# Kernel optimization log

Measured on AMD Instinct MI355X. Metric: run time of the kernel, lower is better.

## Reference

```python
import jax, jax.numpy as jnp
import numpy as np

B, T, D, K = 4, 4096, 256, 16


def hankel_eigvecs(T: int, k: int) -> jnp.ndarray:
    """Top-k |eigenvalue| eigenvectors of Z_ij = 2/((i+j)^3 - (i+j)), 1-indexed."""
    idx = np.arange(1, T + 1, dtype=np.float64)
    ij = idx[None, :] + idx[:, None]
    Z = 2.0 / (ij ** 3 - ij)
    w, v = np.linalg.eigh(Z)
    top = np.argsort(-np.abs(w))[:k]
    return jnp.asarray(v[:, top], dtype=jnp.float32)  # (T, K)


def setup_inputs() -> dict:
    key = jax.random.key(0)
    kx, kw = jax.random.split(key)
    x = jax.random.normal(kx, (B, T, D), dtype=jnp.float32)
    # Stacked weights of the K independent nn.Linear(D, D, bias=False) modules.
    # W[k] is the torch Linear weight (out, in); y = c @ W[k].T.
    W = jax.random.normal(kw, (K, D, D), dtype=jnp.float32) * (1.0 / np.sqrt(D))
    phi = hankel_eigvecs(T, K)  # Hankel eigenvector buffer (non-trainable)
    return {"x": x, "W": W, "phi": phi}


def reference(x, W, phi):
    # x: (B,T,D), W: (K,D,D), phi: (T,K)
    # c_k[t] = cumsum_{s<=t} phi[s,k] * x[s]   -> batched over all K filters
    C = jnp.cumsum(phi[None, :, :, None] * x[:, :, None, :], axis=1)  # (B,T,K,D)
    # out[t] = sum_k phi[t,k] * (c_k[t] @ W_k^T)
    out = jnp.einsum('btkd,ked,tk->bte', C, W, phi)  # (B,T,D)
    return out  # dropout is identity in eval mode (dropout=0.0)
```

## Files before the change

kernel.cpp:

```cpp
#include <hip/hip_runtime.h>


typedef __bf16 bf16x8 __attribute__((ext_vector_type(8)));
typedef float  f32x4  __attribute__((ext_vector_type(4)));
typedef unsigned short u16;

__device__ static inline u16 f2bf(float f) {
    unsigned int u = __float_as_uint(f);
    u = (u + 0x7fffu + ((u >> 16) & 1u)) >> 16;
    return (u16)u;
}

__device__ static inline void gload16(const void* g, void* l) {
    __builtin_amdgcn_global_load_lds((const __attribute__((address_space(1))) void*)g,
                                     (__attribute__((address_space(3))) void*)l, 16, 0, 0);
}

__global__ __launch_bounds__(256) void k0_wt(const float* __restrict__ W, u16* __restrict__ WT) {
    const int e = blockIdx.x, d = threadIdx.x;
    union { u16 u[16]; uint4 v[2]; } ob;
#pragma unroll
    for (int k = 0; k < 16; ++k)
        ob.u[k] = f2bf(W[((size_t)k * 256 + e) * 256 + d]);
    uint4* dst = (uint4*)(WT + (size_t)e * 4096 + d * 16);
    dst[0] = ob.v[0]; dst[1] = ob.v[1];
}

__global__ __launch_bounds__(256) void k1_sums(const float* __restrict__ x,
                                               const float* __restrict__ phi,
                                               float* __restrict__ U) {
    __shared__ float phis[256];
    const int tid = threadIdx.x;
    const int b = blockIdx.x, c = blockIdx.y;
    const int t0 = c * 16;
    phis[tid] = phi[t0 * 16 + tid];
    __syncthreads();
    float acc[16];
#pragma unroll
    for (int k = 0; k < 16; ++k) acc[k] = 0.f;
    for (int s = 0; s < 16; ++s) {
        const float xv = x[(size_t)((b << 12) + t0 + s) * 256 + tid];
        union { float f[16]; float4 v[4]; } pv;
#pragma unroll
        for (int j = 0; j < 4; ++j) pv.v[j] = *(const float4*)&phis[s * 16 + j * 4];
#pragma unroll
        for (int k = 0; k < 16; ++k) acc[k] = fmaf(pv.f[k], xv, acc[k]);
    }
    float4* Up = (float4*)(U + ((size_t)((b * 256 + c) * 256 + tid)) * 16);
    union { float f[16]; float4 v[4]; } ov;
#pragma unroll
    for (int k = 0; k < 16; ++k) ov.f[k] = acc[k];
#pragma unroll
    for (int j = 0; j < 4; ++j) Up[j] = ov.v[j];
}

__global__ __launch_bounds__(256) void k2_scan(float* __restrict__ U) {
    const int b  = blockIdx.x;
    const int dl = threadIdx.x & 63;
    const int dk = blockIdx.y * 64 + dl;
    const int q  = threadIdx.x >> 6;
    float* base = U + (size_t)b * 1048576 + (size_t)(q * 64) * 4096 + dk;
    float s = 0.f;
#pragma unroll 8
    for (int j = 0; j < 64; ++j) s += base[(size_t)j * 4096];
    __shared__ float qs[4][64];
    qs[q][dl] = s;
    __syncthreads();
    float pre = 0.f;
#pragma unroll
    for (int i = 0; i < 4; ++i) pre += (i < q) ? qs[i][dl] : 0.f;
    float run = pre;
#pragma unroll 8
    for (int j = 0; j < 64; ++j) {
        const float v = base[(size_t)j * 4096];
        base[(size_t)j * 4096] = run;
        run += v;
    }
}

__global__ __launch_bounds__(512, 4) void k4_fused(const float* __restrict__ x,
                                                   const float* __restrict__ phi,
                                                   const float* __restrict__ U,
                                                   const u16* __restrict__ BT,
                                                   float* __restrict__ C) {
    __shared__ __align__(16) char smem[81920];
    const int tid = threadIdx.x;
    const int m0 = blockIdx.x * 64;
    const int ks = blockIdx.y;
    const int b  = m0 >> 12, t0 = m0 & 4095, c0 = t0 >> 4;
    const int w = tid >> 6, l = tid & 63;
    const int wm = (w >> 2) * 32, wn = (w & 3) * 64;
    const int lg = l >> 4, lr = l & 15;
    f32x4 acc[2][4] = {};

    float p[16];
    if (w < 4) {
#pragma unroll
        for (int s = 0; s < 16; ++s) p[s] = phi[(t0 + w * 16 + s) * 16 + lr];
    }
    const char* Bb = (const char*)BT;
    const int tl = tid & 255;
    const int colb = (lg * 16 + lr) * 2;

    auto stageB = [&](int kt, int buf) {
        const int kofs = ks * 4096 + kt * 128;
#pragma unroll
        for (int c = 0; c < 8; ++c) {
            const int row = c * 32 + (tl >> 3);
            gload16(Bb + (size_t)row * 8192 + kofs + (((tl & 7) * 16) ^ ((row & 7) << 4)),
                    smem + 16384 + buf * 32768 + c * 4096 + tl * 16);
        }
    };
    auto chains = [&](int kt, int buf) {
        const int d = ks * 128 + kt * 4 + lg;
        float run = U[(((size_t)(b * 256 + c0 + w)) * 256 + d) * 16 + lr];
        char* Ab = smem + buf * 8192 + w * 2048;
#pragma unroll
        for (int s = 0; s < 16; ++s) {
            const float xv = x[(size_t)(m0 + w * 16 + s) * 256 + d];
            run = fmaf(p[s], xv, run);
            *(u16*)(Ab + s * 128 + (colb ^ ((s & 7) << 4))) = f2bf(p[s] * run);
        }
    };

    if (w >= 4) stageB(0, 0); else chains(0, 0);
    __syncthreads();

    for (int kt = 0; kt < 32; ++kt) {
        const int cur = kt & 1;
        if (kt < 31) {
            if (w >= 4) stageB(kt + 1, cur ^ 1);
            else        chains(kt + 1, cur ^ 1);
        }
        const char* Abase = smem + cur * 8192;
        const char* Bbase = smem + 16384 + cur * 32768;
#pragma unroll
        for (int kk = 0; kk < 2; ++kk) {
            const int kb = kk * 64 + lg * 16;
            bf16x8 af[2], bfv[4];
#pragma unroll
            for (int mi = 0; mi < 2; ++mi) {
                const int r = wm + mi * 16 + lr;
                af[mi] = *(const bf16x8*)(Abase + r * 128 + (kb ^ ((r & 7) << 4)));
            }
#pragma unroll
            for (int ni = 0; ni < 4; ++ni) {
                const int n = wn + ni * 16 + lr;
                bfv[ni] = *(const bf16x8*)(Bbase + n * 128 + (kb ^ ((n & 7) << 4)));
            }
#pragma unroll
            for (int mi = 0; mi < 2; ++mi)
#pragma unroll
                for (int ni = 0; ni < 4; ++ni)
                    acc[mi][ni] = __builtin_amdgcn_mfma_f32_16x16x32_bf16(af[mi], bfv[ni], acc[mi][ni], 0, 0, 0);
        }
        __syncthreads();
    }

#pragma unroll
    for (int mi = 0; mi < 2; ++mi)
#pragma unroll
        for (int ni = 0; ni < 4; ++ni)
#pragma unroll
            for (int r = 0; r < 4; ++r) {
                const int row = m0 + wm + mi * 16 + lg * 4 + r;
                const int col = wn + ni * 16 + lr;
                unsafeAtomicAdd(&C[(size_t)row * 256 + col], acc[mi][ni][r]);
            }
}

extern "C" void kernel_launch(void* const* d_in, const int* in_sizes, int n_in,
                              void* d_out, int out_size, void* d_ws, size_t ws_size,
                              hipStream_t stream) {
    const float* x   = (const float*)d_in[0];
    const float* W   = (const float*)d_in[1];
    const float* phi = (const float*)d_in[2];
    float* out = (float*)d_out;

    char* ws = (char*)d_ws;
    u16*   WT = (u16*)ws;
    float* U  = (float*)(ws + (2u << 20));

    k0_wt  <<<256, 256, 0, stream>>>(W, WT);
    k1_sums<<<dim3(4, 256), 256, 0, stream>>>(x, phi, U);
    k2_scan<<<dim3(4, 64), 256, 0, stream>>>(U);
    hipMemsetAsync(d_out, 0, (size_t)out_size * sizeof(float), stream);
    k4_fused<<<dim3(256, 2), 512, 0, stream>>>(x, phi, U, WT, out);
}
```

Before: 98.70 us.

## Drop split-K, triple-buffer B, prefetch x chains and store output directly

Removes the two-way split-K grid so each block computes the full K=4096 reduction, which lets the output be written with plain stores instead of atomics and drops the memset. B tiles are now triple-buffered with manual vmcnt waits and raw barriers. Only two waves build the A chains, each thread handling two filter columns with packed bf16 conversion, and x loads are prefetched two steps ahead in registers. The cost is half the blocks (256), more LDS per block and lower occupancy, and the hand-placed waitcnt and barrier logic is fragile.

```diff
diff --git a/kernel.cpp b/kernel.cpp
--- a/kernel.cpp
+++ b/kernel.cpp
@@ -4,6 +4,7 @@
 typedef __bf16 bf16x8 __attribute__((ext_vector_type(8)));
 typedef float  f32x4  __attribute__((ext_vector_type(4)));
 typedef unsigned short u16;
+typedef unsigned int   u32;
 
 __device__ static inline u16 f2bf(float f) {
     unsigned int u = __float_as_uint(f);
@@ -78,62 +79,67 @@
     }
 }
 
-__global__ __launch_bounds__(512, 4) void k4_fused(const float* __restrict__ x,
+__global__ __launch_bounds__(512, 2) void k4_fused(const float* __restrict__ x,
                                                    const float* __restrict__ phi,
                                                    const float* __restrict__ U,
                                                    const u16* __restrict__ BT,
                                                    float* __restrict__ C) {
-    __shared__ __align__(16) char smem[81920];
+    __shared__ __align__(16) char smem[114688];
     const int tid = threadIdx.x;
     const int m0 = blockIdx.x * 64;
-    const int ks = blockIdx.y;
     const int b  = m0 >> 12, t0 = m0 & 4095, c0 = t0 >> 4;
     const int w = tid >> 6, l = tid & 63;
     const int wm = (w >> 2) * 32, wn = (w & 3) * 64;
     const int lg = l >> 4, lr = l & 15;
     f32x4 acc[2][4] = {};
 
-    float p[16];
-    if (w < 4) {
-#pragma unroll
-        for (int s = 0; s < 16; ++s) p[s] = phi[(t0 + w * 16 + s) * 16 + lr];
-    }
-    const char* Bb = (const char*)BT;
+    const bool is_chain = (w < 2);
+    const bool is_stage = (w >= 4);
+
+    const int kp = l & 7, dl = (l >> 3) & 3, ch = ((w & 1) << 1) | (l >> 5);
+    const int colb = dl * 32 + kp * 4;
+    float2 p01[16];
+    if (is_chain) {
+#pragma unroll
+        for (int s = 0; s < 16; ++s)
+            p01[s] = *(const float2*)&phi[(t0 + ch * 16 + s) * 16 + kp * 2];
+    }
+
     const int tl = tid & 255;
-    const int colb = (lg * 16 + lr) * 2;
-
-    auto stageB = [&](int kt, int buf) {
-        const int kofs = ks * 4096 + kt * 128;
-#pragma unroll
-        for (int c = 0; c < 8; ++c) {
-            const int row = c * 32 + (tl >> 3);
-            gload16(Bb + (size_t)row * 8192 + kofs + (((tl & 7) * 16) ^ ((row & 7) << 4)),
-                    smem + 16384 + buf * 32768 + c * 4096 + tl * 16);
-        }
-    };
-    auto chains = [&](int kt, int buf) {
-        const int d = ks * 128 + kt * 4 + lg;
-        float run = U[(((size_t)(b * 256 + c0 + w)) * 256 + d) * 16 + lr];
-        char* Ab = smem + buf * 8192 + w * 2048;
+    const char* bsrc = (const char*)BT + (size_t)(tl >> 3) * 8192
+                     + (((tl & 7) * 16) ^ (((tl >> 3) & 7) << 4));
+    char* const smemA = smem + 98304;
+
+    auto stageB = [&](int kt, int bufw) {
+        char* dst = smem + bufw * 32768 + tl * 16;
+        const char* src = bsrc + (size_t)kt * 128;
+#pragma unroll
+        for (int c = 0; c < 8; ++c)
+            gload16(src + (size_t)c * 262144, dst + c * 4096);
+    };
+    auto issueX = [&](float (&xr)[16], float2& us, int kt) {
+        const int d = kt * 4 + dl;
+        const float* xp = x + (size_t)(m0 + ch * 16) * 256 + d;
+#pragma unroll
+        for (int s = 0; s < 16; ++s) xr[s] = xp[(size_t)s * 256];
+        us = *(const float2*)&U[((size_t)((b * 256 + c0 + ch) * 256 + d)) * 16 + kp * 2];
+    };
+    auto chains = [&](const float (&xr)[16], float2 us, int abw) {
+        float r0 = us.x, r1 = us.y;
+        char* Ab = smemA + abw * 8192 + ch * 2048;
 #pragma unroll
         for (int s = 0; s < 16; ++s) {
-            const float xv = x[(size_t)(m0 + w * 16 + s) * 256 + d];
-            run = fmaf(p[s], xv, run);
-            *(u16*)(Ab + s * 128 + (colb ^ ((s & 7) << 4))) = f2bf(p[s] * run);
-        }
-    };
-
-    if (w >= 4) stageB(0, 0); else chains(0, 0);
-    __syncthreads();
-
-    for (int kt = 0; kt < 32; ++kt) {
-        const int cur = kt & 1;
-        if (kt < 31) {
-            if (w >= 4) stageB(kt + 1, cur ^ 1);
-            else        chains(kt + 1, cur ^ 1);
-        }
-        const char* Abase = smem + cur * 8192;
-        const char* Bbase = smem + 16384 + cur * 32768;
+            r0 = fmaf(p01[s].x, xr[s], r0);
+            r1 = fmaf(p01[s].y, xr[s], r1);
+            const float v0 = p01[s].x * r0, v1 = p01[s].y * r1;
+            u32 pk;
+            asm("v_cvt_pk_bf16_f32 %0, %1, %2" : "=v"(pk) : "v"(v0), "v"(v1));
+            *(u32*)(Ab + s * 128 + (colb ^ ((s & 7) << 4))) = pk;
+        }
+    };
+    auto mfma_phase = [&](int abr, int bbr) {
+        const char* Abase = smemA + abr * 8192;
+        const char* Bbase = smem + bbr * 32768;
 #pragma unroll
         for (int kk = 0; kk < 2; ++kk) {
             const int kb = kk * 64 + lg * 16;
@@ -154,7 +160,45 @@
                 for (int ni = 0; ni < 4; ++ni)
                     acc[mi][ni] = __builtin_amdgcn_mfma_f32_16x16x32_bf16(af[mi], bfv[ni], acc[mi][ni], 0, 0, 0);
         }
-        __syncthreads();
+    };
+
+    float xA[16], xB[16]; float2 uA, uB;
+    if (is_chain) { issueX(xA, uA, 0); issueX(xB, uB, 1); }
+    if (is_stage) { stageB(0, 0); stageB(1, 1); }
+    __builtin_amdgcn_sched_barrier(0);
+    if (is_chain) {
+        chains(xA, uA, 0);
+        asm volatile("s_waitcnt lgkmcnt(0)" ::: "memory");
+    }
+    if (is_stage) asm volatile("s_waitcnt vmcnt(8)" ::: "memory");
+    asm volatile("s_barrier" ::: "memory");
+
+    int br = 0, bw = 2;
+    auto body = [&](int kt, float (&xW)[16], float2& uW,
+                    const float (&xR)[16], float2 uR) {
+        const int abr = kt & 1;
+        if (kt + 2 < 64) {
+            if (is_stage)      stageB(kt + 2, bw);
+            else if (is_chain) issueX(xW, uW, kt + 2);
+        }
+        __builtin_amdgcn_sched_barrier(0);
+        if (is_chain && (kt + 1 < 64)) chains(xR, uR, abr ^ 1);
+        __builtin_amdgcn_s_setprio(1);
+        mfma_phase(abr, br);
+        __builtin_amdgcn_s_setprio(0);
+        if (is_chain) asm volatile("s_waitcnt lgkmcnt(0)" ::: "memory");
+        if (is_stage) {
+            if (kt + 2 < 64) asm volatile("s_waitcnt vmcnt(8)" ::: "memory");
+            else             asm volatile("s_waitcnt vmcnt(0)" ::: "memory");
+        }
+        if (kt < 63) asm volatile("s_barrier" ::: "memory");
+        br = (br == 2) ? 0 : br + 1;
+        bw = (bw == 2) ? 0 : bw + 1;
+    };
+
+    for (int kt = 0; kt < 64; kt += 2) {
+        body(kt,     xA, uA, xB, uB);
+        body(kt + 1, xB, uB, xA, uA);
     }
 
 #pragma unroll
@@ -165,7 +209,7 @@
             for (int r = 0; r < 4; ++r) {
                 const int row = m0 + wm + mi * 16 + lg * 4 + r;
                 const int col = wn + ni * 16 + lr;
-                unsafeAtomicAdd(&C[(size_t)row * 256 + col], acc[mi][ni][r]);
+                C[(size_t)row * 256 + col] = acc[mi][ni][r];
             }
 }
 
@@ -184,6 +228,5 @@
     k0_wt  <<<256, 256, 0, stream>>>(W, WT);
     k1_sums<<<dim3(4, 256), 256, 0, stream>>>(x, phi, U);
     k2_scan<<<dim3(4, 64), 256, 0, stream>>>(U);
-    hipMemsetAsync(d_out, 0, (size_t)out_size * sizeof(float), stream);
-    k4_fused<<<dim3(256, 2), 512, 0, stream>>>(x, phi, U, WT, out);
-}
+    k4_fused<<<256, 512, 0, stream>>>(x, phi, U, WT, out);
+}
```

Result: faster. 95.44 us (-3.3%).

## Enlarge fused GEMM tile to 256 rows and split K four ways

Applied to the files above, without the earlier changes.

The fused chain+GEMM kernel now handles 256 rows per block instead of 64, and the K dimension is split four ways instead of two. Every wave now does both B staging and chain computation, with each lane computing two filter chains and packing them with v_cvt_pk_bf16_f32. The MFMA phase is raised to high priority with s_setprio. The larger tile lets each staged B tile serve more rows and halves the number of K iterations, at the cost of 128KB LDS, 8x4 accumulators per wave, lower occupancy and more atomic-add traffic from the wider K split.

```diff
diff --git a/kernel.cpp b/kernel.cpp
--- a/kernel.cpp
+++ b/kernel.cpp
@@ -4,6 +4,7 @@
 typedef __bf16 bf16x8 __attribute__((ext_vector_type(8)));
 typedef float  f32x4  __attribute__((ext_vector_type(4)));
 typedef unsigned short u16;
+typedef unsigned int   u32;
 
 __device__ static inline u16 f2bf(float f) {
     unsigned int u = __float_as_uint(f);
@@ -78,87 +79,106 @@
     }
 }
 
-__global__ __launch_bounds__(512, 4) void k4_fused(const float* __restrict__ x,
+__global__ __launch_bounds__(512, 2) void k4_fused(const float* __restrict__ x,
                                                    const float* __restrict__ phi,
                                                    const float* __restrict__ U,
                                                    const u16* __restrict__ BT,
                                                    float* __restrict__ C) {
-    __shared__ __align__(16) char smem[81920];
+    __shared__ __align__(16) char smem[131072];
     const int tid = threadIdx.x;
-    const int m0 = blockIdx.x * 64;
+    const int m0 = blockIdx.x * 256;
     const int ks = blockIdx.y;
     const int b  = m0 >> 12, t0 = m0 & 4095, c0 = t0 >> 4;
     const int w = tid >> 6, l = tid & 63;
-    const int wm = (w >> 2) * 32, wn = (w & 3) * 64;
+    const int wm = (w >> 2) * 128, wn = (w & 3) * 64;
     const int lg = l >> 4, lr = l & 15;
-    f32x4 acc[2][4] = {};
-
-    float p[16];
-    if (w < 4) {
-#pragma unroll
-        for (int s = 0; s < 16; ++s) p[s] = phi[(t0 + w * 16 + s) * 16 + lr];
-    }
-    const char* Bb = (const char*)BT;
-    const int tl = tid & 255;
-    const int colb = (lg * 16 + lr) * 2;
+    f32x4 acc[8][4] = {};
+
+    const int kp = l & 7, dl = (l >> 3) & 3, ch = (w << 1) | (l >> 5);
+    const int colb = dl * 32 + kp * 4;
+    float2 p01[16];
+#pragma unroll
+    for (int s = 0; s < 16; ++s)
+        p01[s] = *(const float2*)&phi[(t0 + ch * 16 + s) * 16 + kp * 2];
+
+    const char* bsrc = (const char*)BT + (size_t)(tid >> 3) * 8192 + ks * 2048
+                     + (((tid & 7) * 16) ^ (((tid >> 3) & 7) << 4));
+    char* const smemA = smem + 65536;
 
     auto stageB = [&](int kt, int buf) {
-        const int kofs = ks * 4096 + kt * 128;
-#pragma unroll
-        for (int c = 0; c < 8; ++c) {
-            const int row = c * 32 + (tl >> 3);
-            gload16(Bb + (size_t)row * 8192 + kofs + (((tl & 7) * 16) ^ ((row & 7) << 4)),
-                    smem + 16384 + buf * 32768 + c * 4096 + tl * 16);
+        char* dst = smem + buf * 32768 + tid * 16;
+        const char* src = bsrc + (size_t)kt * 128;
+#pragma unroll
+        for (int c = 0; c < 4; ++c)
+            gload16(src + (size_t)c * 524288, dst + c * 8192);
+    };
+    auto chains = [&](int kt, int buf) {
+        const int d = ks * 64 + kt * 4 + dl;
+        const float* xp = x + (size_t)(m0 + ch * 16) * 256 + d;
+        const float2 us = *(const float2*)&U[((size_t)((b * 256 + c0 + ch) * 256 + d)) * 16 + kp * 2];
+        float xr[16];
+#pragma unroll
+        for (int s = 0; s < 16; ++s) xr[s] = xp[(size_t)s * 256];
+        float r0 = us.x, r1 = us.y;
+        char* Ab = smemA + buf * 32768 + (ch * 16) * 128;
+#pragma unroll
+        for (int s = 0; s < 16; ++s) {
+            r0 = fmaf(p01[s].x, xr[s], r0);
+            r1 = fmaf(p01[s].y, xr[s], r1);
+            const float v0 = p01[s].x * r0, v1 = p01[s].y * r1;
+            u32 pk;
+            asm("v_cvt_pk_bf16_f32 %0, %1, %2" : "=v"(pk) : "v"(v0), "v"(v1));
+            *(u32*)(Ab + s * 128 + (colb ^ ((s & 7) << 4))) = pk;
         }
     };
-    auto chains = [&](int kt, int buf) {
-        const int d = ks * 128 + kt * 4 + lg;
-        float run = U[(((size_t)(b * 256 + c0 + w)) * 256 + d) * 16 + lr];
-        char* Ab = smem + buf * 8192 + w * 2048;
-#pragma unroll
-        for (int s = 0; s < 16; ++s) {
-            const float xv = x[(size_t)(m0 + w * 16 + s) * 256 + d];
-            run = fmaf(p[s], xv, run);
-            *(u16*)(Ab + s * 128 + (colb ^ ((s & 7) << 4))) = f2bf(p[s] * run);
-        }
-    };
-
-    if (w >= 4) stageB(0, 0); else chains(0, 0);
-    __syncthreads();
-
-    for (int kt = 0; kt < 32; ++kt) {
-        const int cur = kt & 1;
-        if (kt < 31) {
-            if (w >= 4) stageB(kt + 1, cur ^ 1);
-            else        chains(kt + 1, cur ^ 1);
-        }
-        const char* Abase = smem + cur * 8192;
-        const char* Bbase = smem + 16384 + cur * 32768;
+    auto mfma_phase = [&](int buf) {
+        const char* Abase = smemA + buf * 32768;
+        const char* Bbase = smem + buf * 32768;
 #pragma unroll
         for (int kk = 0; kk < 2; ++kk) {
             const int kb = kk * 64 + lg * 16;
-            bf16x8 af[2], bfv[4];
-#pragma unroll
-            for (int mi = 0; mi < 2; ++mi) {
-                const int r = wm + mi * 16 + lr;
-                af[mi] = *(const bf16x8*)(Abase + r * 128 + (kb ^ ((r & 7) << 4)));
-            }
+            bf16x8 bfv[4];
 #pragma unroll
             for (int ni = 0; ni < 4; ++ni) {
                 const int n = wn + ni * 16 + lr;
                 bfv[ni] = *(const bf16x8*)(Bbase + n * 128 + (kb ^ ((n & 7) << 4)));
             }
 #pragma unroll
-            for (int mi = 0; mi < 2; ++mi)
-#pragma unroll
-                for (int ni = 0; ni < 4; ++ni)
-                    acc[mi][ni] = __builtin_amdgcn_mfma_f32_16x16x32_bf16(af[mi], bfv[ni], acc[mi][ni], 0, 0, 0);
+            for (int mh = 0; mh < 2; ++mh) {
+                bf16x8 af[4];
+#pragma unroll
+                for (int mi = 0; mi < 4; ++mi) {
+                    const int r = wm + (mh * 4 + mi) * 16 + lr;
+                    af[mi] = *(const bf16x8*)(Abase + r * 128 + (kb ^ ((r & 7) << 4)));
+                }
+#pragma unroll
+                for (int mi = 0; mi < 4; ++mi)
+#pragma unroll
+                    for (int ni = 0; ni < 4; ++ni)
+                        acc[mh * 4 + mi][ni] = __builtin_amdgcn_mfma_f32_16x16x32_bf16(
+                            af[mi], bfv[ni], acc[mh * 4 + mi][ni], 0, 0, 0);
+            }
         }
+    };
+
+    stageB(0, 0);
+    chains(0, 0);
+    __syncthreads();
+
+    for (int kt = 0; kt < 16; ++kt) {
+        const int cur = kt & 1;
+        if (kt < 15) {
+            stageB(kt + 1, cur ^ 1);
+            chains(kt + 1, cur ^ 1);
+        }
+        __builtin_amdgcn_s_setprio(1);
+        mfma_phase(cur);
+        __builtin_amdgcn_s_setprio(0);
         __syncthreads();
     }
 
 #pragma unroll
-    for (int mi = 0; mi < 2; ++mi)
+    for (int mi = 0; mi < 8; ++mi)
 #pragma unroll
         for (int ni = 0; ni < 4; ++ni)
 #pragma unroll
@@ -185,5 +205,5 @@
     k1_sums<<<dim3(4, 256), 256, 0, stream>>>(x, phi, U);
     k2_scan<<<dim3(4, 64), 256, 0, stream>>>(U);
     hipMemsetAsync(d_out, 0, (size_t)out_size * sizeof(float), stream);
-    k4_fused<<<dim3(256, 2), 512, 0, stream>>>(x, phi, U, WT, out);
-}
+    k4_fused<<<dim3(64, 4), 512, 0, stream>>>(x, phi, U, WT, out);
+}
```

New measurement: 120.2 us. 21.7% more time.
